# Kernel tuning notes

Measured on AMD Instinct MI355X. Metric: run time of the kernel, lower is better.

The kernel has to match this reference:

```python
import jax, jax.numpy as jnp
import numpy as np

N_ATOMS = 65536
N_BONDS = 131072
N_MOLS = 512
D_IN = 16
D = 128
REPEAT = 3


def _dense(key, fan_in, fan_out):
    kw, kb = jax.random.split(key)
    scale = 1.0 / np.sqrt(fan_in)
    W = jax.random.normal(kw, (fan_in, fan_out), dtype=jnp.float32) * scale
    b = jnp.zeros((fan_out,), dtype=jnp.float32)
    return W, b


def setup_inputs() -> dict:
    key = jax.random.key(0)
    ks = jax.random.split(key, 12)
    atoms = jax.random.normal(ks[0], (N_ATOMS, D_IN), dtype=jnp.float32)
    bond_orders = jax.random.uniform(ks[1], (N_BONDS,), dtype=jnp.float32)
    bond_src = jax.random.randint(ks[2], (N_BONDS,), 0, N_ATOMS, dtype=jnp.int32)
    bond_dst = jax.random.randint(ks[3], (N_BONDS,), 0, N_ATOMS, dtype=jnp.int32)
    atom_mol = jnp.sort(jax.random.randint(ks[4], (N_ATOMS,), 0, N_MOLS, dtype=jnp.int32))
    bond_mol = jnp.sort(jax.random.randint(ks[5], (N_BONDS,), 0, N_MOLS, dtype=jnp.int32))
    W_fe, b_fe = _dense(ks[6], 1, D)      # f_e : bond order -> h_e
    W_fv, b_fv = _dense(ks[7], D_IN, D)   # f_v : atom feats -> h_v
    W_fu, b_fu = _dense(ks[8], D, D)      # f_u : per-mol init from aggregated nodes
    W_e, b_e = _dense(ks[9], 5 * D, D)    # phi_e(h_e, h_e0, h_left, h_right, u)
    W_v, b_v = _dense(ks[10], 4 * D, D)   # phi_v(h_v, h_v0, e_bar_i, u)
    W_u, b_u = _dense(ks[11], 4 * D, D)   # phi_u(h_u, h_u0, e_bar, v_bar)
    return dict(atoms=atoms, bond_orders=bond_orders, W_fe=W_fe, b_fe=b_fe,
                W_fv=W_fv, b_fv=b_fv, W_fu=W_fu, b_fu=b_fu, W_e=W_e, b_e=b_e,
                W_v=W_v, b_v=b_v, W_u=W_u, b_u=b_u,
                bond_src=bond_src, bond_dst=bond_dst,
                atom_mol=atom_mol, bond_mol=bond_mol)


def reference(atoms, bond_orders, W_fe, b_fe, W_fv, b_fv, W_fu, b_fu,
              W_e, b_e, W_v, b_v, W_u, b_u,
              bond_src, bond_dst, atom_mol, bond_mol):
    seg = lambda x, ids, n: jax.ops.segment_sum(x, ids, num_segments=n)
    relu = jax.nn.relu

    # f_e / f_v / f_u initial embeddings
    h_e0 = relu(bond_orders[:, None] @ W_fe + b_fe)           # [E, D]
    h_v0 = relu(atoms @ W_fv + b_fv)                          # [N, D]
    h_u0 = relu(seg(h_v0, atom_mol, N_MOLS) @ W_fu + b_fu)    # [M, D]

    h_e, h_v, h_u = h_e0, h_v0, h_u0
    for _ in range(REPEAT):
        # phi_e(e_k, e_k_0, v_rk, v_sk, u): gather endpoints and per-bond global
        h_left = h_v[bond_src]                                # [E, D]
        h_right = h_v[bond_dst]                               # [E, D]
        u_e = h_u[bond_mol]                                   # [E, D]
        h_e = relu(jnp.concatenate([h_e, h_e0, h_left, h_right, u_e], axis=1) @ W_e + b_e)
        # rho_e_v: sum of updated edges incident to each atom (one-hot mask == scatter-add)
        e_bar_i = seg(h_e, bond_src, N_ATOMS) + seg(h_e, bond_dst, N_ATOMS)  # [N, D]
        # phi_v(v_i, v_i_0, e_bar_i, u)
        h_v = relu(jnp.concatenate([h_v, h_v0, e_bar_i, h_u[atom_mol]], axis=1) @ W_v + b_v)
        # rho_e_u / rho_v_u: per-molecule segment sums
        e_bar = seg(h_e, bond_mol, N_MOLS)                    # [M, D]
        v_bar = seg(h_v, atom_mol, N_MOLS)                    # [M, D]
        # phi_u(u, u_0, e_bar, v_bar)
        h_u = relu(jnp.concatenate([h_u, h_u0, e_bar, v_bar], axis=1) @ W_u + b_u)
    return h_u
```

## Files before the change

### kernel.cpp

```cpp
#include <hip/hip_runtime.h>
#include <hip/hip_bf16.h>
#include <stdint.h>

#define N_ATOMS 65536
#define N_BONDS 131072
#define N_MOLS  512
#define D_IN    16
#define DD      128
#define REPEAT  3
#define PITCH   136

typedef __attribute__((ext_vector_type(8))) short s8b;
typedef __attribute__((ext_vector_type(4))) float f32x4;

__device__ __forceinline__ float us2f(unsigned short s) {
    unsigned int u = ((unsigned int)s) << 16;
    float f; __builtin_memcpy(&f, &u, 4); return f;
}
__device__ __forceinline__ unsigned short f2us(float f) {
    __hip_bfloat16 h = __float2bfloat16(f);
    unsigned short s; __builtin_memcpy(&s, &h, 2); return s;
}
__device__ __forceinline__ void acc8(float* a, uint4 v) {
    unsigned short w[8]; __builtin_memcpy(w, &v, 16);
#pragma unroll
    for (int j = 0; j < 8; j++) a[j] += us2f(w[j]);
}


__device__ __forceinline__ void pack_one(const float* W, unsigned short* Wpk, int idx) {
    int k = idx >> 7, n = idx & 127;
    int c = k >> 7, ks = (k >> 5) & 3, quad = (k >> 3) & 3, j = k & 7;
    Wpk[(((c * 4 + ks) * 4 + quad) * 128 + n) * 8 + j] = f2us(W[k * 128 + n]);
}
__global__ void k_pack2(const float* __restrict__ We, const float* __restrict__ Wv,
                        unsigned short* __restrict__ WeP, unsigned short* __restrict__ WvP) {
    int idx = blockIdx.x * 256 + threadIdx.x;
    const int NE = 640 * 128;
    if (idx < NE) pack_one(We, WeP, idx);
    else if (idx < NE + 512 * 128) pack_one(Wv, WvP, idx - NE);
}

__global__ void k_deg(const int* __restrict__ bsrc, const int* __restrict__ bdst,
                      int* __restrict__ deg) {
    int e = blockIdx.x * 256 + threadIdx.x;
    atomicAdd(&deg[bsrc[e]], 1);
    atomicAdd(&deg[bdst[e]], 1);
}

__global__ void k_scan1(const int* __restrict__ deg, int* __restrict__ bsum) {
    __shared__ int red[256];
    int t = threadIdx.x;
    red[t] = deg[blockIdx.x * 256 + t];
    __syncthreads();
    for (int s = 128; s > 0; s >>= 1) {
        if (t < s) red[t] += red[t + s];
        __syncthreads();
    }
    if (t == 0) bsum[blockIdx.x] = red[0];
}

__global__ void k_scan3b(const int* __restrict__ deg, const int* __restrict__ bsum,
                         int* __restrict__ rowptr, int* __restrict__ cursor) {
    __shared__ int sb[256];
    __shared__ int s[256];
    int t = threadIdx.x;
    sb[t] = bsum[t];
    __syncthreads();
    for (int off = 1; off < 256; off <<= 1) {
        int v = (t >= off) ? sb[t - off] : 0;
        __syncthreads();
        sb[t] += v;
        __syncthreads();
    }
    int boff = sb[blockIdx.x] - bsum[blockIdx.x];
    int i = blockIdx.x * 256 + t;
    int d = deg[i];
    s[t] = d;
    __syncthreads();
    for (int off = 1; off < 256; off <<= 1) {
        int v = (t >= off) ? s[t - off] : 0;
        __syncthreads();
        s[t] += v;
        __syncthreads();
    }
    int val = boff + s[t] - d;
    rowptr[i] = val;
    cursor[i] = val;
    if (i == N_ATOMS - 1) rowptr[N_ATOMS] = val + d;
}

__global__ void k_fill(const int* __restrict__ bsrc, const int* __restrict__ bdst,
                       int* __restrict__ cursor, int* __restrict__ adj) {
    int e = blockIdx.x * 256 + threadIdx.x;
    int p = atomicAdd(&cursor[bsrc[e]], 1); adj[p] = e;
    int q = atomicAdd(&cursor[bdst[e]], 1); adj[q] = e;
}

__global__ void k_molptr2(const int* __restrict__ bmol, const int* __restrict__ amol,
                          int* __restrict__ bptr, int* __restrict__ aptr) {
    int m = threadIdx.x;
    if (m > N_MOLS) return;
    const int* ids = blockIdx.x ? amol : bmol;
    int rows = blockIdx.x ? N_ATOMS : N_BONDS;
    int* out = blockIdx.x ? aptr : bptr;
    int lo = 0, hi = rows;
    while (lo < hi) {
        int mid = (lo + hi) >> 1;
        if (ids[mid] < m) lo = mid + 1; else hi = mid;
    }
    out[m] = lo;
}


__global__ __launch_bounds__(256) void k_molsum_s(const unsigned short* __restrict__ x,
                                                  const int* __restrict__ mptr,
                                                  float* __restrict__ out, int S) {
    __shared__ float red[16 * 128];
    int m = blockIdx.x / S, s = blockIdx.x - m * S;
    int b = mptr[m], e = mptr[m + 1];
    int len = (e - b + S - 1) / S;
    int r0 = b + s * len;
    int r1 = min(r0 + len, e);
    int rl = threadIdx.x >> 4, g = threadIdx.x & 15;
    float acc[8] = {0,0,0,0,0,0,0,0};
    for (int r = r0 + rl; r < r1; r += 16)
        acc8(acc, *reinterpret_cast<const uint4*>(x + (size_t)r * DD + g * 8));
#pragma unroll
    for (int j = 0; j < 8; j++) red[rl * 128 + g * 8 + j] = acc[j];
    __syncthreads();
    if (threadIdx.x < 128) {
        int col = threadIdx.x;
        float sum = 0.f;
#pragma unroll
        for (int i = 0; i < 16; i++) sum += red[i * 128 + col];
        atomicAdd(&out[(size_t)m * DD + col], sum);
    }
}

__global__ __launch_bounds__(256) void k_mol_init_f(
        const float* __restrict__ ns, const float* __restrict__ Wfu,
        const float* __restrict__ bfu,
        const float* __restrict__ We, const float* __restrict__ be,
        const float* __restrict__ Wv, const float* __restrict__ bv,
        float* __restrict__ hu0, float* __restrict__ yue, float* __restrict__ yuv) {
    __shared__ float hrow[2 * DD];
    int tid = threadIdx.x;
    int ml = tid >> 7, d = tid & 127;
    int m = blockIdx.x * 2 + ml;
    float acc = bfu[d];
    for (int k = 0; k < DD; k++)
        acc = fmaf(ns[m*DD + k], Wfu[k*DD + d], acc);
    float v = fmaxf(acc, 0.f);
    hu0[m*DD + d] = v;
    hrow[ml*DD + d] = v;
    __syncthreads();
    float ae = be[d], av = bv[d];
    for (int k = 0; k < DD; k++) {
        float h = hrow[ml*DD + k];
        ae = fmaf(h, We[(512 + k)*DD + d], ae);
        av = fmaf(h, Wv[(384 + k)*DD + d], av);
    }
    yue[m*DD + d] = ae;
    yuv[m*DD + d] = av;
}

__global__ __launch_bounds__(256) void k_ye0(
        const float* __restrict__ bo, const float* __restrict__ Wfe,
        const float* __restrict__ bfe, const unsigned short* __restrict__ Wpk,
        unsigned short* __restrict__ he, unsigned short* __restrict__ ye0) {
    __shared__ __align__(16) unsigned short xs[128 * PITCH];
    __shared__ float sbo[128];
    int tid = threadIdx.x;
    int e0 = blockIdx.x * 128;
    if (tid < 128) sbo[tid] = bo[e0 + tid];
    int wv = tid >> 6, lane = tid & 63, quad = lane >> 4, l15 = lane & 15;
    f32x4 acc[8][2];
#pragma unroll
    for (int mt = 0; mt < 8; mt++) {
        acc[mt][0] = (f32x4){0.f,0.f,0.f,0.f};
        acc[mt][1] = (f32x4){0.f,0.f,0.f,0.f};
    }
    __syncthreads();
    for (int t = 0; t < 8; t++) {
        int u = tid + t * 256;
        int i = u >> 4, g = (u & 15) * 8;
        float b = sbo[i];
        unsigned short tmp[8];
#pragma unroll
        for (int j = 0; j < 8; j++)
            tmp[j] = f2us(fmaxf(fmaf(b, Wfe[g + j], bfe[g + j]), 0.f));
        uint4 val; __builtin_memcpy(&val, tmp, 16);
        *reinterpret_cast<uint4*>(&xs[i * PITCH + g]) = val;
        *reinterpret_cast<uint4*>(he + (size_t)(e0 + i) * DD + g) = val;
    }
    __syncthreads();
#pragma unroll
    for (int ks = 0; ks < 4; ks++) {
        const unsigned short* wb = Wpk + ((1 * 4 + ks) * 4 + quad) * 1024 + (wv * 32 + l15) * 8;
        s8b b0 = *reinterpret_cast<const s8b*>(wb);
        s8b b1 = *reinterpret_cast<const s8b*>(wb + 128);
#pragma unroll
        for (int mt = 0; mt < 8; mt++) {
            s8b afr = *reinterpret_cast<const s8b*>(&xs[(mt*16 + l15) * PITCH + ks*32 + quad*8]);
            acc[mt][0] = __builtin_amdgcn_mfma_f32_16x16x32_bf16(afr, b0, acc[mt][0], 0, 0, 0);
            acc[mt][1] = __builtin_amdgcn_mfma_f32_16x16x32_bf16(afr, b1, acc[mt][1], 0, 0, 0);
        }
    }
#pragma unroll
    for (int mt = 0; mt < 8; mt++)
#pragma unroll
        for (int r = 0; r < 4; r++) {
            int row = e0 + mt*16 + quad*4 + r;
#pragma unroll
            for (int nt = 0; nt < 2; nt++) {
                int col = wv*32 + nt*16 + l15;
                ye0[(size_t)row * DD + col] = f2us(acc[mt][nt][r]);
            }
        }
}

__global__ __launch_bounds__(256) void k_nodes_f(
        const float* __restrict__ atoms, const float* __restrict__ Wfv,
        const float* __restrict__ bfv, const unsigned short* __restrict__ Wpk,
        unsigned short* __restrict__ hv, unsigned short* __restrict__ yv0,
        float* __restrict__ node_sum) {
    __shared__ __align__(16) unsigned short xs[128 * PITCH];
    int tid = threadIdx.x;
    int gid = blockIdx.x * 256 + tid;
    if (gid < N_MOLS * DD) node_sum[gid] = 0.f;
    int n0 = blockIdx.x * 128;
    int wv = tid >> 6, lane = tid & 63, quad = lane >> 4, l15 = lane & 15;
    f32x4 acc[8][2];
#pragma unroll
    for (int mt = 0; mt < 8; mt++) {
        acc[mt][0] = (f32x4){0.f,0.f,0.f,0.f};
        acc[mt][1] = (f32x4){0.f,0.f,0.f,0.f};
    }
    for (int t = 0; t < 8; t++) {
        int u = tid + t * 256;
        int i = u >> 4, g = (u & 15) * 8;
        int row = n0 + i;
        float a[D_IN];
#pragma unroll
        for (int k = 0; k < D_IN; k++) a[k] = atoms[(size_t)row * D_IN + k];
        unsigned short tmp[8];
#pragma unroll
        for (int j = 0; j < 8; j++) {
            float acc1 = bfv[g + j];
#pragma unroll
            for (int k = 0; k < D_IN; k++)
                acc1 = fmaf(a[k], Wfv[k*DD + g + j], acc1);
            tmp[j] = f2us(fmaxf(acc1, 0.f));
        }
        uint4 val; __builtin_memcpy(&val, tmp, 16);
        *reinterpret_cast<uint4*>(&xs[i * PITCH + g]) = val;
        *reinterpret_cast<uint4*>(hv + (size_t)row * DD + g) = val;
    }
    __syncthreads();
#pragma unroll
    for (int ks = 0; ks < 4; ks++) {
        const unsigned short* wb = Wpk + ((1 * 4 + ks) * 4 + quad) * 1024 + (wv * 32 + l15) * 8;
        s8b b0 = *reinterpret_cast<const s8b*>(wb);
        s8b b1 = *reinterpret_cast<const s8b*>(wb + 128);
#pragma unroll
        for (int mt = 0; mt < 8; mt++) {
            s8b afr = *reinterpret_cast<const s8b*>(&xs[(mt*16 + l15) * PITCH + ks*32 + quad*8]);
            acc[mt][0] = __builtin_amdgcn_mfma_f32_16x16x32_bf16(afr, b0, acc[mt][0], 0, 0, 0);
            acc[mt][1] = __builtin_amdgcn_mfma_f32_16x16x32_bf16(afr, b1, acc[mt][1], 0, 0, 0);
        }
    }
#pragma unroll
    for (int mt = 0; mt < 8; mt++)
#pragma unroll
        for (int r = 0; r < 4; r++) {
            int row = n0 + mt*16 + quad*4 + r;
#pragma unroll
            for (int nt = 0; nt < 2; nt++) {
                int col = wv*32 + nt*16 + l15;
                yv0[(size_t)row * DD + col] = f2us(acc[mt][nt][r]);
            }
        }
}

__global__ __launch_bounds__(256) void k_zsd(
        const unsigned short* __restrict__ hv, const unsigned short* __restrict__ Wpk,
        unsigned short* __restrict__ Zs, unsigned short* __restrict__ Zd,
        float* __restrict__ ebar, float* __restrict__ vbar) {
    __shared__ __align__(16) unsigned short xs[128 * PITCH];
    int tid = threadIdx.x;
    int gid = blockIdx.x * 256 + tid;
    if (gid < N_MOLS * DD) ebar[gid] = 0.f;
    else                   vbar[gid - N_MOLS * DD] = 0.f;
    int n0 = blockIdx.x * 128;
    int wv = tid >> 6, lane = tid & 63, quad = lane >> 4, l15 = lane & 15;
    f32x4 aS[8][2], aD[8][2];
#pragma unroll
    for (int mt = 0; mt < 8; mt++) {
        aS[mt][0] = (f32x4){0.f,0.f,0.f,0.f}; aS[mt][1] = (f32x4){0.f,0.f,0.f,0.f};
        aD[mt][0] = (f32x4){0.f,0.f,0.f,0.f}; aD[mt][1] = (f32x4){0.f,0.f,0.f,0.f};
    }
    for (int t = 0; t < 8; t++) {
        int u = tid + t * 256;
        int i = u >> 4, g = (u & 15) * 8;
        *reinterpret_cast<uint4*>(&xs[i * PITCH + g]) =
            *reinterpret_cast<const uint4*>(hv + (size_t)(n0 + i) * DD + g);
    }
    __syncthreads();
#pragma unroll
    for (int ks = 0; ks < 4; ks++) {
        const unsigned short* wbS = Wpk + ((2 * 4 + ks) * 4 + quad) * 1024 + (wv * 32 + l15) * 8;
        const unsigned short* wbD = Wpk + ((3 * 4 + ks) * 4 + quad) * 1024 + (wv * 32 + l15) * 8;
        s8b s0 = *reinterpret_cast<const s8b*>(wbS);
        s8b s1 = *reinterpret_cast<const s8b*>(wbS + 128);
        s8b d0 = *reinterpret_cast<const s8b*>(wbD);
        s8b d1 = *reinterpret_cast<const s8b*>(wbD + 128);
#pragma unroll
        for (int mt = 0; mt < 8; mt++) {
            s8b afr = *reinterpret_cast<const s8b*>(&xs[(mt*16 + l15) * PITCH + ks*32 + quad*8]);
            aS[mt][0] = __builtin_amdgcn_mfma_f32_16x16x32_bf16(afr, s0, aS[mt][0], 0, 0, 0);
            aS[mt][1] = __builtin_amdgcn_mfma_f32_16x16x32_bf16(afr, s1, aS[mt][1], 0, 0, 0);
            aD[mt][0] = __builtin_amdgcn_mfma_f32_16x16x32_bf16(afr, d0, aD[mt][0], 0, 0, 0);
            aD[mt][1] = __builtin_amdgcn_mfma_f32_16x16x32_bf16(afr, d1, aD[mt][1], 0, 0, 0);
        }
    }
#pragma unroll
    for (int mt = 0; mt < 8; mt++)
#pragma unroll
        for (int r = 0; r < 4; r++) {
            int row = n0 + mt*16 + quad*4 + r;
#pragma unroll
            for (int nt = 0; nt < 2; nt++) {
                int col = wv*32 + nt*16 + l15;
                Zs[(size_t)row * DD + col] = f2us(aS[mt][nt][r]);
                Zd[(size_t)row * DD + col] = f2us(aD[mt][nt][r]);
            }
        }
}

__global__ __launch_bounds__(256) void k_phi_e(
        unsigned short* __restrict__ he, const unsigned short* __restrict__ ye0,
        const unsigned short* __restrict__ Zs, const unsigned short* __restrict__ Zd,
        const unsigned short* __restrict__ Wpk, const float* __restrict__ yue,
        const int* __restrict__ bsrc, const int* __restrict__ bdst,
        const int* __restrict__ bmol, float* __restrict__ ebar) {
    __shared__ __align__(16) unsigned short xs[128 * PITCH];
    __shared__ int ssrc[128], sdst[128], smol[128];
    int tid = threadIdx.x;
    int e0 = blockIdx.x * 128;
    if (tid < 128) {
        ssrc[tid] = bsrc[e0 + tid];
        sdst[tid] = bdst[e0 + tid];
        smol[tid] = bmol[e0 + tid];
    }
    int wv = tid >> 6, lane = tid & 63, quad = lane >> 4, l15 = lane & 15;
    f32x4 acc[8][2];
#pragma unroll
    for (int mt = 0; mt < 8; mt++) {
        acc[mt][0] = (f32x4){0.f,0.f,0.f,0.f};
        acc[mt][1] = (f32x4){0.f,0.f,0.f,0.f};
    }
    for (int t = 0; t < 8; t++) {
        int u = tid + t * 256;
        int i = u >> 4, g = (u & 15) * 8;
        *reinterpret_cast<uint4*>(&xs[i * PITCH + g]) =
            *reinterpret_cast<const uint4*>(he + (size_t)(e0 + i) * DD + g);
    }
    __syncthreads();
#pragma unroll
    for (int ks = 0; ks < 4; ks++) {
        const unsigned short* wb = Wpk + ((0 * 4 + ks) * 4 + quad) * 1024 + (wv * 32 + l15) * 8;
        s8b b0 = *reinterpret_cast<const s8b*>(wb);
        s8b b1 = *reinterpret_cast<const s8b*>(wb + 128);
#pragma unroll
        for (int mt = 0; mt < 8; mt++) {
            s8b afr = *reinterpret_cast<const s8b*>(&xs[(mt*16 + l15) * PITCH + ks*32 + quad*8]);
            acc[mt][0] = __builtin_amdgcn_mfma_f32_16x16x32_bf16(afr, b0, acc[mt][0], 0, 0, 0);
            acc[mt][1] = __builtin_amdgcn_mfma_f32_16x16x32_bf16(afr, b1, acc[mt][1], 0, 0, 0);
        }
    }
    __syncthreads();
    for (int t = 0; t < 8; t++) {
        int u = tid + t * 256;
        int i = u >> 4, g = (u & 15) * 8;
        float s[8] = {0,0,0,0,0,0,0,0};
        acc8(s, *reinterpret_cast<const uint4*>(ye0 + (size_t)(e0 + i) * DD + g));
        acc8(s, *reinterpret_cast<const uint4*>(Zs  + (size_t)ssrc[i] * DD + g));
        acc8(s, *reinterpret_cast<const uint4*>(Zd  + (size_t)sdst[i] * DD + g));
        const float* yr = yue + (size_t)smol[i] * DD + g;
        float4 y0 = *reinterpret_cast<const float4*>(yr);
        float4 y1 = *reinterpret_cast<const float4*>(yr + 4);
        s[0] += y0.x; s[1] += y0.y; s[2] += y0.z; s[3] += y0.w;
        s[4] += y1.x; s[5] += y1.y; s[6] += y1.z; s[7] += y1.w;
        unsigned short tmp[8];
#pragma unroll
        for (int j = 0; j < 8; j++) tmp[j] = f2us(s[j]);
        uint4 val; __builtin_memcpy(&val, tmp, 16);
        *reinterpret_cast<uint4*>(&xs[i * PITCH + g]) = val;
    }
    __syncthreads();
#pragma unroll
    for (int nt = 0; nt < 2; nt++) {
        int col = wv*32 + nt*16 + l15;
        float run = 0.f;
        int cur = smol[quad * 4];
#pragma unroll
        for (int mt = 0; mt < 8; mt++)
#pragma unroll
            for (int r = 0; r < 4; r++) {
                int rl = mt*16 + quad*4 + r;
                float v = fmaxf(acc[mt][nt][r] + us2f(xs[rl * PITCH + col]), 0.f);
                he[(size_t)(e0 + rl) * DD + col] = f2us(v);
                int m = smol[rl];
                if (m != cur) { atomicAdd(&ebar[(size_t)cur * DD + col], run); run = 0.f; cur = m; }
                run += v;
            }
        atomicAdd(&ebar[(size_t)cur * DD + col], run);
    }
}

__global__ __launch_bounds__(256) void k_phi_v(
        unsigned short* __restrict__ hv, const unsigned short* __restrict__ he,
        const int* __restrict__ rowptr, const int* __restrict__ adj,
        const unsigned short* __restrict__ yv0,
        const unsigned short* __restrict__ Wpk, const float* __restrict__ yuv,
        const int* __restrict__ amol, float* __restrict__ vbar) {
    __shared__ __align__(16) unsigned short xs[128 * PITCH];
    __shared__ int smol[128];
    int tid = threadIdx.x;
    int n0 = blockIdx.x * 128;
    if (tid < 128) smol[tid] = amol[n0 + tid];
    int wv = tid >> 6, lane = tid & 63, quad = lane >> 4, l15 = lane & 15;
    f32x4 acc[8][2];
#pragma unroll
    for (int mt = 0; mt < 8; mt++) {
        acc[mt][0] = (f32x4){0.f,0.f,0.f,0.f};
        acc[mt][1] = (f32x4){0.f,0.f,0.f,0.f};
    }
    for (int t = 0; t < 8; t++) {
        int u = tid + t * 256;
        int i = u >> 4, g = (u & 15) * 8;
        *reinterpret_cast<uint4*>(&xs[i * PITCH + g]) =
            *reinterpret_cast<const uint4*>(hv + (size_t)(n0 + i) * DD + g);
    }
    __syncthreads();
#pragma unroll
    for (int ks = 0; ks < 4; ks++) {
        const unsigned short* wb = Wpk + ((0 * 4 + ks) * 4 + quad) * 1024 + (wv * 32 + l15) * 8;
        s8b b0 = *reinterpret_cast<const s8b*>(wb);
        s8b b1 = *reinterpret_cast<const s8b*>(wb + 128);
#pragma unroll
        for (int mt = 0; mt < 8; mt++) {
            s8b afr = *reinterpret_cast<const s8b*>(&xs[(mt*16 + l15) * PITCH + ks*32 + quad*8]);
            acc[mt][0] = __builtin_amdgcn_mfma_f32_16x16x32_bf16(afr, b0, acc[mt][0], 0, 0, 0);
            acc[mt][1] = __builtin_amdgcn_mfma_f32_16x16x32_bf16(afr, b1, acc[mt][1], 0, 0, 0);
        }
    }
    __syncthreads();
    {
        int g = tid & 15, ab = tid >> 4;
#pragma unroll
        for (int k = 0; k < 8; k++) {
            int a = ab + 16 * k;
            int n = n0 + a;
            int b = rowptr[n], e = rowptr[n + 1];
            float s[8] = {0,0,0,0,0,0,0,0};
            int j = b;
            for (; j + 1 < e; j += 2) {
                uint4 v0 = *reinterpret_cast<const uint4*>(he + (size_t)adj[j]     * DD + g * 8);
                uint4 v1 = *reinterpret_cast<const uint4*>(he + (size_t)adj[j + 1] * DD + g * 8);
                acc8(s, v0); acc8(s, v1);
            }
            if (j < e)
                acc8(s, *reinterpret_cast<const uint4*>(he + (size_t)adj[j] * DD + g * 8));
            unsigned short tmp[8];
#pragma unroll
            for (int jj = 0; jj < 8; jj++) tmp[jj] = f2us(s[jj]);
            uint4 val; __builtin_memcpy(&val, tmp, 16);
            *reinterpret_cast<uint4*>(&xs[a * PITCH + g * 8]) = val;
        }
    }
    __syncthreads();
#pragma unroll
    for (int ks = 0; ks < 4; ks++) {
        const unsigned short* wb = Wpk + ((2 * 4 + ks) * 4 + quad) * 1024 + (wv * 32 + l15) * 8;
        s8b b0 = *reinterpret_cast<const s8b*>(wb);
        s8b b1 = *reinterpret_cast<const s8b*>(wb + 128);
#pragma unroll
        for (int mt = 0; mt < 8; mt++) {
            s8b afr = *reinterpret_cast<const s8b*>(&xs[(mt*16 + l15) * PITCH + ks*32 + quad*8]);
            acc[mt][0] = __builtin_amdgcn_mfma_f32_16x16x32_bf16(afr, b0, acc[mt][0], 0, 0, 0);
            acc[mt][1] = __builtin_amdgcn_mfma_f32_16x16x32_bf16(afr, b1, acc[mt][1], 0, 0, 0);
        }
    }
    __syncthreads();
    for (int t = 0; t < 8; t++) {
        int u = tid + t * 256;
        int i = u >> 4, g = (u & 15) * 8;
        float s[8] = {0,0,0,0,0,0,0,0};
        acc8(s, *reinterpret_cast<const uint4*>(yv0 + (size_t)(n0 + i) * DD + g));
        const float* yr = yuv + (size_t)smol[i] * DD + g;
        float4 y0 = *reinterpret_cast<const float4*>(yr);
        float4 y1 = *reinterpret_cast<const float4*>(yr + 4);
        s[0] += y0.x; s[1] += y0.y; s[2] += y0.z; s[3] += y0.w;
        s[4] += y1.x; s[5] += y1.y; s[6] += y1.z; s[7] += y1.w;
        unsigned short tmp[8];
#pragma unroll
        for (int j = 0; j < 8; j++) tmp[j] = f2us(s[j]);
        uint4 val; __builtin_memcpy(&val, tmp, 16);
        *reinterpret_cast<uint4*>(&xs[i * PITCH + g]) = val;
    }
    __syncthreads();
#pragma unroll
    for (int nt = 0; nt < 2; nt++) {
        int col = wv*32 + nt*16 + l15;
        float run = 0.f;
        int cur = smol[quad * 4];
#pragma unroll
        for (int mt = 0; mt < 8; mt++)
#pragma unroll
            for (int r = 0; r < 4; r++) {
                int rl = mt*16 + quad*4 + r;
                float v = fmaxf(acc[mt][nt][r] + us2f(xs[rl * PITCH + col]), 0.f);
                hv[(size_t)(n0 + rl) * DD + col] = f2us(v);
                int m = smol[rl];
                if (m != cur) { atomicAdd(&vbar[(size_t)cur * DD + col], run); run = 0.f; cur = m; }
                run += v;
            }
        atomicAdd(&vbar[(size_t)cur * DD + col], run);
    }
}

__global__ __launch_bounds__(256) void k_phi_u_f(
        const float* __restrict__ hu_in, const float* __restrict__ hu0,
        const float* __restrict__ ebar, const float* __restrict__ vbar,
        const float* __restrict__ Wu, const float* __restrict__ bu,
        const float* __restrict__ We, const float* __restrict__ be,
        const float* __restrict__ Wv, const float* __restrict__ bv,
        float* __restrict__ hu_out, float* __restrict__ dout,
        float* __restrict__ yue, float* __restrict__ yuv) {
    __shared__ float hrow[2 * DD];
    int tid = threadIdx.x;
    int ml = tid >> 7, d = tid & 127;
    int m = blockIdx.x * 2 + ml;
    float acc = bu[d];
    const float* segs[4] = { hu_in + m*DD, hu0 + m*DD, ebar + m*DD, vbar + m*DD };
    for (int s = 0; s < 4; s++) {
        const float* x = segs[s];
        const float* W = Wu + (s*DD)*DD + d;
        for (int k = 0; k < DD; k++)
            acc = fmaf(x[k], W[k*DD], acc);
    }
    float v = fmaxf(acc, 0.f);
    hu_out[m*DD + d] = v;
    dout[m*DD + d] = v;
    hrow[ml*DD + d] = v;
    __syncthreads();
    float ae = be[d], av = bv[d];
    for (int k = 0; k < DD; k++) {
        float h = hrow[ml*DD + k];
        ae = fmaf(h, We[(512 + k)*DD + d], ae);
        av = fmaf(h, Wv[(384 + k)*DD + d], av);
    }
    yue[m*DD + d] = ae;
    yuv[m*DD + d] = av;
}


extern "C" void kernel_launch(void* const* d_in, const int* in_sizes, int n_in,
                              void* d_out, int out_size, void* d_ws, size_t ws_size,
                              hipStream_t stream) {
    const float* atoms = (const float*)d_in[0];
    const float* bo    = (const float*)d_in[1];
    const float* Wfe   = (const float*)d_in[2];
    const float* bfe   = (const float*)d_in[3];
    const float* Wfv   = (const float*)d_in[4];
    const float* bfv   = (const float*)d_in[5];
    const float* Wfu   = (const float*)d_in[6];
    const float* bfu   = (const float*)d_in[7];
    const float* We    = (const float*)d_in[8];
    const float* be    = (const float*)d_in[9];
    const float* Wv    = (const float*)d_in[10];
    const float* bv    = (const float*)d_in[11];
    const float* Wu    = (const float*)d_in[12];
    const float* bu    = (const float*)d_in[13];
    const int* bsrc    = (const int*)d_in[14];
    const int* bdst    = (const int*)d_in[15];
    const int* amol    = (const int*)d_in[16];
    const int* bmol    = (const int*)d_in[17];

    char* p = (char*)d_ws;
    auto alloc = [&](size_t bytes) {
        char* r = p;
        p += (bytes + 255) & ~(size_t)255;
        return r;
    };
    unsigned short* he     = (unsigned short*)alloc((size_t)N_BONDS * DD * 2);
    unsigned short* ye0    = (unsigned short*)alloc((size_t)N_BONDS * DD * 2);
    unsigned short* hv     = (unsigned short*)alloc((size_t)N_ATOMS * DD * 2);
    unsigned short* yv0    = (unsigned short*)alloc((size_t)N_ATOMS * DD * 2);
    unsigned short* Zs     = (unsigned short*)alloc((size_t)N_ATOMS * DD * 2);
    unsigned short* Zd     = (unsigned short*)alloc((size_t)N_ATOMS * DD * 2);
    unsigned short* WeP    = (unsigned short*)alloc((size_t)640 * DD * 2);
    unsigned short* WvP    = (unsigned short*)alloc((size_t)512 * DD * 2);
    int* deg      = (int*)alloc((size_t)N_ATOMS * 4);
    int* rowptr   = (int*)alloc((size_t)(N_ATOMS + 1) * 4);
    int* cursor   = (int*)alloc((size_t)N_ATOMS * 4);
    int* adj      = (int*)alloc((size_t)2 * N_BONDS * 4);
    int* bmol_ptr = (int*)alloc((size_t)(N_MOLS + 1) * 4);
    int* amol_ptr = (int*)alloc((size_t)(N_MOLS + 1) * 4);
    int* bsum     = (int*)alloc((size_t)256 * 4);
    float* node_sum = (float*)alloc((size_t)N_MOLS * DD * 4);
    float* hu0   = (float*)alloc((size_t)N_MOLS * DD * 4);
    float* huA   = (float*)alloc((size_t)N_MOLS * DD * 4);
    float* huB   = (float*)alloc((size_t)N_MOLS * DD * 4);
    float* ebar  = (float*)alloc((size_t)N_MOLS * DD * 4);
    float* vbar  = (float*)alloc((size_t)N_MOLS * DD * 4);
    float* yue   = (float*)alloc((size_t)N_MOLS * DD * 4);
    float* yuv   = (float*)alloc((size_t)N_MOLS * DD * 4);

    hipMemsetAsync(deg, 0, (size_t)N_ATOMS * 4, stream);
    k_deg<<<N_BONDS/256, 256, 0, stream>>>(bsrc, bdst, deg);
    k_scan1<<<256, 256, 0, stream>>>(deg, bsum);
    k_scan3b<<<256, 256, 0, stream>>>(deg, bsum, rowptr, cursor);
    k_fill<<<N_BONDS/256, 256, 0, stream>>>(bsrc, bdst, cursor, adj);
    k_molptr2<<<2, 1024, 0, stream>>>(bmol, amol, bmol_ptr, amol_ptr);

    k_pack2<<<(640*DD + 512*DD)/256, 256, 0, stream>>>(We, Wv, WeP, WvP);

    k_ye0<<<N_BONDS/128, 256, 0, stream>>>(bo, Wfe, bfe, WeP, he, ye0);
    k_nodes_f<<<N_ATOMS/128, 256, 0, stream>>>(atoms, Wfv, bfv, WvP, hv, yv0, node_sum);
    k_molsum_s<<<N_MOLS*2, 256, 0, stream>>>(hv, amol_ptr, node_sum, 2);
    k_mol_init_f<<<N_MOLS/2, 256, 0, stream>>>(node_sum, Wfu, bfu, We, be, Wv, bv,
                                               hu0, yue, yuv);

    const float* hu_in = hu0; float* hu_out = huA;

    for (int r = 0; r < REPEAT; r++) {
        k_zsd<<<N_ATOMS/128, 256, 0, stream>>>(hv, WeP, Zs, Zd, ebar, vbar);
        k_phi_e<<<N_BONDS/128, 256, 0, stream>>>(he, ye0, Zs, Zd, WeP, yue,
                                                 bsrc, bdst, bmol, ebar);
        k_phi_v<<<N_ATOMS/128, 256, 0, stream>>>(hv, he, rowptr, adj, yv0, WvP, yuv,
                                                 amol, vbar);
        k_phi_u_f<<<N_MOLS/2, 256, 0, stream>>>(hu_in, hu0, ebar, vbar, Wu, bu,
                                                We, be, Wv, bv,
                                                hu_out, (float*)d_out, yue, yuv);
        hu_in = hu_out; hu_out = (hu_out == huA) ? huB : huA;
    }
}
```

Baseline: 537.7 us.

## Fuse Zs/Zd projection into node kernels, recompute ye0 in phi_e, split edge aggregation

Drops the separate k_zsd kernel: the source/destination projections of h_v are computed in k_nodes_f for the first iteration and at the end of k_phi_v for later ones, reusing the h_v tile already in shared memory. The stored ye0 buffer is removed; k_phi_e recomputes h_e0 from bond orders and runs an extra MFMA pass, trading compute for 32 MB of reads per iteration. The per-atom incident-edge sum moves into its own k_ebar kernel with 4-way unrolled gathers, and k_phi_v now reads that bf16 result. The ebar/vbar zeroing moves into the molecule kernels.

Result: faster. 498.6 us (-7.3%).

```diff
diff --git a/kernel.cpp b/kernel.cpp
--- a/kernel.cpp
+++ b/kernel.cpp
@@ -25,6 +25,41 @@
     unsigned short w[8]; __builtin_memcpy(w, &v, 16);
 #pragma unroll
     for (int j = 0; j < 8; j++) a[j] += us2f(w[j]);
+}
+
+__device__ __forceinline__ void mfma_store(const unsigned short* xs,
+        const unsigned short* __restrict__ Wpk, int wc,
+        unsigned short* __restrict__ out, int row0, int tid) {
+    int wv = tid >> 6, lane = tid & 63, quad = lane >> 4, l15 = lane & 15;
+    f32x4 acc[8][2];
+#pragma unroll
+    for (int mt = 0; mt < 8; mt++) {
+        acc[mt][0] = (f32x4){0.f,0.f,0.f,0.f};
+        acc[mt][1] = (f32x4){0.f,0.f,0.f,0.f};
+    }
+#pragma unroll
+    for (int ks = 0; ks < 4; ks++) {
+        const unsigned short* wb = Wpk + ((wc * 4 + ks) * 4 + quad) * 1024 + (wv * 32 + l15) * 8;
+        s8b b0 = *reinterpret_cast<const s8b*>(wb);
+        s8b b1 = *reinterpret_cast<const s8b*>(wb + 128);
+#pragma unroll
+        for (int mt = 0; mt < 8; mt++) {
+            s8b afr = *reinterpret_cast<const s8b*>(&xs[(mt*16 + l15) * PITCH + ks*32 + quad*8]);
+            acc[mt][0] = __builtin_amdgcn_mfma_f32_16x16x32_bf16(afr, b0, acc[mt][0], 0, 0, 0);
+            acc[mt][1] = __builtin_amdgcn_mfma_f32_16x16x32_bf16(afr, b1, acc[mt][1], 0, 0, 0);
+        }
+    }
+#pragma unroll
+    for (int mt = 0; mt < 8; mt++)
+#pragma unroll
+        for (int r = 0; r < 4; r++) {
+            int row = row0 + mt*16 + quad*4 + r;
+#pragma unroll
+            for (int nt = 0; nt < 2; nt++) {
+                int col = wv*32 + nt*16 + l15;
+                out[(size_t)row * DD + col] = f2us(acc[mt][nt][r]);
+            }
+        }
 }
 
 
@@ -112,6 +147,51 @@
     out[m] = lo;
 }
 
+
+__global__ void k_init_he(const float* __restrict__ bo, const float* __restrict__ Wfe,
+                          const float* __restrict__ bfe, unsigned short* __restrict__ he) {
+    int idx = blockIdx.x * 256 + threadIdx.x;
+    int e = idx >> 7, d = idx & 127;
+    he[idx] = f2us(fmaxf(fmaf(bo[e], Wfe[d], bfe[d]), 0.f));
+}
+
+__global__ __launch_bounds__(256) void k_nodes_f(
+        const float* __restrict__ atoms, const float* __restrict__ Wfv,
+        const float* __restrict__ bfv,
+        const unsigned short* __restrict__ WvP, const unsigned short* __restrict__ WeP,
+        unsigned short* __restrict__ hv, unsigned short* __restrict__ yv0,
+        unsigned short* __restrict__ Zs, unsigned short* __restrict__ Zd,
+        float* __restrict__ node_sum) {
+    __shared__ __align__(16) unsigned short xs[128 * PITCH];
+    int tid = threadIdx.x;
+    int gid = blockIdx.x * 256 + tid;
+    if (gid < N_MOLS * DD) node_sum[gid] = 0.f;
+    int n0 = blockIdx.x * 128;
+    for (int t = 0; t < 8; t++) {
+        int u = tid + t * 256;
+        int i = u >> 4, g = (u & 15) * 8;
+        int row = n0 + i;
+        float a[D_IN];
+#pragma unroll
+        for (int k = 0; k < D_IN; k++) a[k] = atoms[(size_t)row * D_IN + k];
+        unsigned short tmp[8];
+#pragma unroll
+        for (int j = 0; j < 8; j++) {
+            float acc1 = bfv[g + j];
+#pragma unroll
+            for (int k = 0; k < D_IN; k++)
+                acc1 = fmaf(a[k], Wfv[k*DD + g + j], acc1);
+            tmp[j] = f2us(fmaxf(acc1, 0.f));
+        }
+        uint4 val; __builtin_memcpy(&val, tmp, 16);
+        *reinterpret_cast<uint4*>(&xs[i * PITCH + g]) = val;
+        *reinterpret_cast<uint4*>(hv + (size_t)row * DD + g) = val;
+    }
+    __syncthreads();
+    mfma_store(xs, WvP, 1, yv0, n0, tid);
+    mfma_store(xs, WeP, 2, Zs, n0, tid);
+    mfma_store(xs, WeP, 3, Zd, n0, tid);
+}
 
 __global__ __launch_bounds__(256) void k_molsum_s(const unsigned short* __restrict__ x,
                                                   const int* __restrict__ mptr,
@@ -143,11 +223,14 @@
         const float* __restrict__ bfu,
         const float* __restrict__ We, const float* __restrict__ be,
         const float* __restrict__ Wv, const float* __restrict__ bv,
-        float* __restrict__ hu0, float* __restrict__ yue, float* __restrict__ yuv) {
+        float* __restrict__ hu0, float* __restrict__ yue, float* __restrict__ yuv,
+        float* __restrict__ ebar, float* __restrict__ vbar) {
     __shared__ float hrow[2 * DD];
     int tid = threadIdx.x;
     int ml = tid >> 7, d = tid & 127;
     int m = blockIdx.x * 2 + ml;
+    ebar[m*DD + d] = 0.f;
+    vbar[m*DD + d] = 0.f;
     float acc = bfu[d];
     for (int k = 0; k < DD; k++)
         acc = fmaf(ns[m*DD + k], Wfu[k*DD + d], acc);
@@ -165,193 +248,24 @@
     yuv[m*DD + d] = av;
 }
 
-__global__ __launch_bounds__(256) void k_ye0(
+__global__ __launch_bounds__(256) void k_phi_e(
+        unsigned short* __restrict__ he,
         const float* __restrict__ bo, const float* __restrict__ Wfe,
-        const float* __restrict__ bfe, const unsigned short* __restrict__ Wpk,
-        unsigned short* __restrict__ he, unsigned short* __restrict__ ye0) {
-    __shared__ __align__(16) unsigned short xs[128 * PITCH];
-    __shared__ float sbo[128];
-    int tid = threadIdx.x;
-    int e0 = blockIdx.x * 128;
-    if (tid < 128) sbo[tid] = bo[e0 + tid];
-    int wv = tid >> 6, lane = tid & 63, quad = lane >> 4, l15 = lane & 15;
-    f32x4 acc[8][2];
-#pragma unroll
-    for (int mt = 0; mt < 8; mt++) {
-        acc[mt][0] = (f32x4){0.f,0.f,0.f,0.f};
-        acc[mt][1] = (f32x4){0.f,0.f,0.f,0.f};
-    }
-    __syncthreads();
-    for (int t = 0; t < 8; t++) {
-        int u = tid + t * 256;
-        int i = u >> 4, g = (u & 15) * 8;
-        float b = sbo[i];
-        unsigned short tmp[8];
-#pragma unroll
-        for (int j = 0; j < 8; j++)
-            tmp[j] = f2us(fmaxf(fmaf(b, Wfe[g + j], bfe[g + j]), 0.f));
-        uint4 val; __builtin_memcpy(&val, tmp, 16);
-        *reinterpret_cast<uint4*>(&xs[i * PITCH + g]) = val;
-        *reinterpret_cast<uint4*>(he + (size_t)(e0 + i) * DD + g) = val;
-    }
-    __syncthreads();
-#pragma unroll
-    for (int ks = 0; ks < 4; ks++) {
-        const unsigned short* wb = Wpk + ((1 * 4 + ks) * 4 + quad) * 1024 + (wv * 32 + l15) * 8;
-        s8b b0 = *reinterpret_cast<const s8b*>(wb);
-        s8b b1 = *reinterpret_cast<const s8b*>(wb + 128);
-#pragma unroll
-        for (int mt = 0; mt < 8; mt++) {
-            s8b afr = *reinterpret_cast<const s8b*>(&xs[(mt*16 + l15) * PITCH + ks*32 + quad*8]);
-            acc[mt][0] = __builtin_amdgcn_mfma_f32_16x16x32_bf16(afr, b0, acc[mt][0], 0, 0, 0);
-            acc[mt][1] = __builtin_amdgcn_mfma_f32_16x16x32_bf16(afr, b1, acc[mt][1], 0, 0, 0);
-        }
-    }
-#pragma unroll
-    for (int mt = 0; mt < 8; mt++)
-#pragma unroll
-        for (int r = 0; r < 4; r++) {
-            int row = e0 + mt*16 + quad*4 + r;
-#pragma unroll
-            for (int nt = 0; nt < 2; nt++) {
-                int col = wv*32 + nt*16 + l15;
-                ye0[(size_t)row * DD + col] = f2us(acc[mt][nt][r]);
-            }
-        }
-}
-
-__global__ __launch_bounds__(256) void k_nodes_f(
-        const float* __restrict__ atoms, const float* __restrict__ Wfv,
-        const float* __restrict__ bfv, const unsigned short* __restrict__ Wpk,
-        unsigned short* __restrict__ hv, unsigned short* __restrict__ yv0,
-        float* __restrict__ node_sum) {
-    __shared__ __align__(16) unsigned short xs[128 * PITCH];
-    int tid = threadIdx.x;
-    int gid = blockIdx.x * 256 + tid;
-    if (gid < N_MOLS * DD) node_sum[gid] = 0.f;
-    int n0 = blockIdx.x * 128;
-    int wv = tid >> 6, lane = tid & 63, quad = lane >> 4, l15 = lane & 15;
-    f32x4 acc[8][2];
-#pragma unroll
-    for (int mt = 0; mt < 8; mt++) {
-        acc[mt][0] = (f32x4){0.f,0.f,0.f,0.f};
-        acc[mt][1] = (f32x4){0.f,0.f,0.f,0.f};
-    }
-    for (int t = 0; t < 8; t++) {
-        int u = tid + t * 256;
-        int i = u >> 4, g = (u & 15) * 8;
-        int row = n0 + i;
-        float a[D_IN];
-#pragma unroll
-        for (int k = 0; k < D_IN; k++) a[k] = atoms[(size_t)row * D_IN + k];
-        unsigned short tmp[8];
-#pragma unroll
-        for (int j = 0; j < 8; j++) {
-            float acc1 = bfv[g + j];
-#pragma unroll
-            for (int k = 0; k < D_IN; k++)
-                acc1 = fmaf(a[k], Wfv[k*DD + g + j], acc1);
-            tmp[j] = f2us(fmaxf(acc1, 0.f));
-        }
-        uint4 val; __builtin_memcpy(&val, tmp, 16);
-        *reinterpret_cast<uint4*>(&xs[i * PITCH + g]) = val;
-        *reinterpret_cast<uint4*>(hv + (size_t)row * DD + g) = val;
-    }
-    __syncthreads();
-#pragma unroll
-    for (int ks = 0; ks < 4; ks++) {
-        const unsigned short* wb = Wpk + ((1 * 4 + ks) * 4 + quad) * 1024 + (wv * 32 + l15) * 8;
-        s8b b0 = *reinterpret_cast<const s8b*>(wb);
-        s8b b1 = *reinterpret_cast<const s8b*>(wb + 128);
-#pragma unroll
-        for (int mt = 0; mt < 8; mt++) {
-            s8b afr = *reinterpret_cast<const s8b*>(&xs[(mt*16 + l15) * PITCH + ks*32 + quad*8]);
-            acc[mt][0] = __builtin_amdgcn_mfma_f32_16x16x32_bf16(afr, b0, acc[mt][0], 0, 0, 0);
-            acc[mt][1] = __builtin_amdgcn_mfma_f32_16x16x32_bf16(afr, b1, acc[mt][1], 0, 0, 0);
-        }
-    }
-#pragma unroll
-    for (int mt = 0; mt < 8; mt++)
-#pragma unroll
-        for (int r = 0; r < 4; r++) {
-            int row = n0 + mt*16 + quad*4 + r;
-#pragma unroll
-            for (int nt = 0; nt < 2; nt++) {
-                int col = wv*32 + nt*16 + l15;
-                yv0[(size_t)row * DD + col] = f2us(acc[mt][nt][r]);
-            }
-        }
-}
-
-__global__ __launch_bounds__(256) void k_zsd(
-        const unsigned short* __restrict__ hv, const unsigned short* __restrict__ Wpk,
-        unsigned short* __restrict__ Zs, unsigned short* __restrict__ Zd,
-        float* __restrict__ ebar, float* __restrict__ vbar) {
-    __shared__ __align__(16) unsigned short xs[128 * PITCH];
-    int tid = threadIdx.x;
-    int gid = blockIdx.x * 256 + tid;
-    if (gid < N_MOLS * DD) ebar[gid] = 0.f;
-    else                   vbar[gid - N_MOLS * DD] = 0.f;
-    int n0 = blockIdx.x * 128;
-    int wv = tid >> 6, lane = tid & 63, quad = lane >> 4, l15 = lane & 15;
-    f32x4 aS[8][2], aD[8][2];
-#pragma unroll
-    for (int mt = 0; mt < 8; mt++) {
-        aS[mt][0] = (f32x4){0.f,0.f,0.f,0.f}; aS[mt][1] = (f32x4){0.f,0.f,0.f,0.f};
-        aD[mt][0] = (f32x4){0.f,0.f,0.f,0.f}; aD[mt][1] = (f32x4){0.f,0.f,0.f,0.f};
-    }
-    for (int t = 0; t < 8; t++) {
-        int u = tid + t * 256;
-        int i = u >> 4, g = (u & 15) * 8;
-        *reinterpret_cast<uint4*>(&xs[i * PITCH + g]) =
-            *reinterpret_cast<const uint4*>(hv + (size_t)(n0 + i) * DD + g);
-    }
-    __syncthreads();
-#pragma unroll
-    for (int ks = 0; ks < 4; ks++) {
-        const unsigned short* wbS = Wpk + ((2 * 4 + ks) * 4 + quad) * 1024 + (wv * 32 + l15) * 8;
-        const unsigned short* wbD = Wpk + ((3 * 4 + ks) * 4 + quad) * 1024 + (wv * 32 + l15) * 8;
-        s8b s0 = *reinterpret_cast<const s8b*>(wbS);
-        s8b s1 = *reinterpret_cast<const s8b*>(wbS + 128);
-        s8b d0 = *reinterpret_cast<const s8b*>(wbD);
-        s8b d1 = *reinterpret_cast<const s8b*>(wbD + 128);
-#pragma unroll
-        for (int mt = 0; mt < 8; mt++) {
-            s8b afr = *reinterpret_cast<const s8b*>(&xs[(mt*16 + l15) * PITCH + ks*32 + quad*8]);
-            aS[mt][0] = __builtin_amdgcn_mfma_f32_16x16x32_bf16(afr, s0, aS[mt][0], 0, 0, 0);
-            aS[mt][1] = __builtin_amdgcn_mfma_f32_16x16x32_bf16(afr, s1, aS[mt][1], 0, 0, 0);
-            aD[mt][0] = __builtin_amdgcn_mfma_f32_16x16x32_bf16(afr, d0, aD[mt][0], 0, 0, 0);
-            aD[mt][1] = __builtin_amdgcn_mfma_f32_16x16x32_bf16(afr, d1, aD[mt][1], 0, 0, 0);
-        }
-    }
-#pragma unroll
-    for (int mt = 0; mt < 8; mt++)
-#pragma unroll
-        for (int r = 0; r < 4; r++) {
-            int row = n0 + mt*16 + quad*4 + r;
-#pragma unroll
-            for (int nt = 0; nt < 2; nt++) {
-                int col = wv*32 + nt*16 + l15;
-                Zs[(size_t)row * DD + col] = f2us(aS[mt][nt][r]);
-                Zd[(size_t)row * DD + col] = f2us(aD[mt][nt][r]);
-            }
-        }
-}
-
-__global__ __launch_bounds__(256) void k_phi_e(
-        unsigned short* __restrict__ he, const unsigned short* __restrict__ ye0,
+        const float* __restrict__ bfe,
         const unsigned short* __restrict__ Zs, const unsigned short* __restrict__ Zd,
         const unsigned short* __restrict__ Wpk, const float* __restrict__ yue,
         const int* __restrict__ bsrc, const int* __restrict__ bdst,
         const int* __restrict__ bmol, float* __restrict__ ebar) {
     __shared__ __align__(16) unsigned short xs[128 * PITCH];
     __shared__ int ssrc[128], sdst[128], smol[128];
+    __shared__ float sbo[128];
     int tid = threadIdx.x;
     int e0 = blockIdx.x * 128;
     if (tid < 128) {
         ssrc[tid] = bsrc[e0 + tid];
         sdst[tid] = bdst[e0 + tid];
         smol[tid] = bmol[e0 + tid];
+        sbo[tid]  = bo[e0 + tid];
     }
     int wv = tid >> 6, lane = tid & 63, quad = lane >> 4, l15 = lane & 15;
     f32x4 acc[8][2];
@@ -383,10 +297,34 @@
     for (int t = 0; t < 8; t++) {
         int u = tid + t * 256;
         int i = u >> 4, g = (u & 15) * 8;
+        float b = sbo[i];
+        unsigned short tmp[8];
+#pragma unroll
+        for (int j = 0; j < 8; j++)
+            tmp[j] = f2us(fmaxf(fmaf(b, Wfe[g + j], bfe[g + j]), 0.f));
+        uint4 val; __builtin_memcpy(&val, tmp, 16);
+        *reinterpret_cast<uint4*>(&xs[i * PITCH + g]) = val;
+    }
+    __syncthreads();
+#pragma unroll
+    for (int ks = 0; ks < 4; ks++) {
+        const unsigned short* wb = Wpk + ((1 * 4 + ks) * 4 + quad) * 1024 + (wv * 32 + l15) * 8;
+        s8b b0 = *reinterpret_cast<const s8b*>(wb);
+        s8b b1 = *reinterpret_cast<const s8b*>(wb + 128);
+#pragma unroll
+        for (int mt = 0; mt < 8; mt++) {
+            s8b afr = *reinterpret_cast<const s8b*>(&xs[(mt*16 + l15) * PITCH + ks*32 + quad*8]);
+            acc[mt][0] = __builtin_amdgcn_mfma_f32_16x16x32_bf16(afr, b0, acc[mt][0], 0, 0, 0);
+            acc[mt][1] = __builtin_amdgcn_mfma_f32_16x16x32_bf16(afr, b1, acc[mt][1], 0, 0, 0);
+        }
+    }
+    __syncthreads();
+    for (int t = 0; t < 8; t++) {
+        int u = tid + t * 256;
+        int i = u >> 4, g = (u & 15) * 8;
         float s[8] = {0,0,0,0,0,0,0,0};
-        acc8(s, *reinterpret_cast<const uint4*>(ye0 + (size_t)(e0 + i) * DD + g));
-        acc8(s, *reinterpret_cast<const uint4*>(Zs  + (size_t)ssrc[i] * DD + g));
-        acc8(s, *reinterpret_cast<const uint4*>(Zd  + (size_t)sdst[i] * DD + g));
+        acc8(s, *reinterpret_cast<const uint4*>(Zs + (size_t)ssrc[i] * DD + g));
+        acc8(s, *reinterpret_cast<const uint4*>(Zd + (size_t)sdst[i] * DD + g));
         const float* yr = yue + (size_t)smol[i] * DD + g;
         float4 y0 = *reinterpret_cast<const float4*>(yr);
         float4 y1 = *reinterpret_cast<const float4*>(yr + 4);
@@ -419,12 +357,38 @@
     }
 }
 
+__global__ __launch_bounds__(256) void k_ebar(const unsigned short* __restrict__ he,
+                                              const int* __restrict__ rowptr,
+                                              const int* __restrict__ adj,
+                                              unsigned short* __restrict__ ebar_i) {
+    int n = blockIdx.x * 16 + (threadIdx.x >> 4);
+    int g = threadIdx.x & 15;
+    int b = rowptr[n], e = rowptr[n + 1];
+    float acc[8] = {0,0,0,0,0,0,0,0};
+    int j = b;
+    for (; j + 3 < e; j += 4) {
+        uint4 v0 = *reinterpret_cast<const uint4*>(he + (size_t)adj[j]     * DD + g * 8);
+        uint4 v1 = *reinterpret_cast<const uint4*>(he + (size_t)adj[j + 1] * DD + g * 8);
+        uint4 v2 = *reinterpret_cast<const uint4*>(he + (size_t)adj[j + 2] * DD + g * 8);
+        uint4 v3 = *reinterpret_cast<const uint4*>(he + (size_t)adj[j + 3] * DD + g * 8);
+        acc8(acc, v0); acc8(acc, v1); acc8(acc, v2); acc8(acc, v3);
+    }
+    for (; j < e; j++)
+        acc8(acc, *reinterpret_cast<const uint4*>(he + (size_t)adj[j] * DD + g * 8));
+    unsigned short o[8];
+#pragma unroll
+    for (int k = 0; k < 8; k++) o[k] = f2us(acc[k]);
+    uint4 ov; __builtin_memcpy(&ov, o, 16);
+    *reinterpret_cast<uint4*>(ebar_i + (size_t)n * DD + g * 8) = ov;
+}
+
 __global__ __launch_bounds__(256) void k_phi_v(
-        unsigned short* __restrict__ hv, const unsigned short* __restrict__ he,
-        const int* __restrict__ rowptr, const int* __restrict__ adj,
+        unsigned short* __restrict__ hv, const unsigned short* __restrict__ ebar_i,
         const unsigned short* __restrict__ yv0,
-        const unsigned short* __restrict__ Wpk, const float* __restrict__ yuv,
-        const int* __restrict__ amol, float* __restrict__ vbar) {
+        const unsigned short* __restrict__ WvP, const unsigned short* __restrict__ WeP,
+        const float* __restrict__ yuv, const int* __restrict__ amol,
+        float* __restrict__ vbar,
+        unsigned short* __restrict__ Zs, unsigned short* __restrict__ Zd, int do_z) {
     __shared__ __align__(16) unsigned short xs[128 * PITCH];
     __shared__ int smol[128];
     int tid = threadIdx.x;
@@ -437,60 +401,29 @@
         acc[mt][0] = (f32x4){0.f,0.f,0.f,0.f};
         acc[mt][1] = (f32x4){0.f,0.f,0.f,0.f};
     }
-    for (int t = 0; t < 8; t++) {
-        int u = tid + t * 256;
-        int i = u >> 4, g = (u & 15) * 8;
-        *reinterpret_cast<uint4*>(&xs[i * PITCH + g]) =
-            *reinterpret_cast<const uint4*>(hv + (size_t)(n0 + i) * DD + g);
-    }
-    __syncthreads();
-#pragma unroll
-    for (int ks = 0; ks < 4; ks++) {
-        const unsigned short* wb = Wpk + ((0 * 4 + ks) * 4 + quad) * 1024 + (wv * 32 + l15) * 8;
-        s8b b0 = *reinterpret_cast<const s8b*>(wb);
-        s8b b1 = *reinterpret_cast<const s8b*>(wb + 128);
-#pragma unroll
-        for (int mt = 0; mt < 8; mt++) {
-            s8b afr = *reinterpret_cast<const s8b*>(&xs[(mt*16 + l15) * PITCH + ks*32 + quad*8]);
-            acc[mt][0] = __builtin_amdgcn_mfma_f32_16x16x32_bf16(afr, b0, acc[mt][0], 0, 0, 0);
-            acc[mt][1] = __builtin_amdgcn_mfma_f32_16x16x32_bf16(afr, b1, acc[mt][1], 0, 0, 0);
-        }
-    }
-    __syncthreads();
-    {
-        int g = tid & 15, ab = tid >> 4;
-#pragma unroll
-        for (int k = 0; k < 8; k++) {
-            int a = ab + 16 * k;
-            int n = n0 + a;
-            int b = rowptr[n], e = rowptr[n + 1];
-            float s[8] = {0,0,0,0,0,0,0,0};
-            int j = b;
-            for (; j + 1 < e; j += 2) {
-                uint4 v0 = *reinterpret_cast<const uint4*>(he + (size_t)adj[j]     * DD + g * 8);
-                uint4 v1 = *reinterpret_cast<const uint4*>(he + (size_t)adj[j + 1] * DD + g * 8);
-                acc8(s, v0); acc8(s, v1);
+    const unsigned short* bases[2] = { hv + (size_t)n0 * DD, ebar_i + (size_t)n0 * DD };
+    const int wcs[2] = {0, 2};
+    for (int c = 0; c < 2; c++) {
+        if (c) __syncthreads();
+        for (int t = 0; t < 8; t++) {
+            int u = tid + t * 256;
+            int i = u >> 4, g = (u & 15) * 8;
+            *reinterpret_cast<uint4*>(&xs[i * PITCH + g]) =
+                *reinterpret_cast<const uint4*>(bases[c] + (size_t)i * DD + g);
+        }
+        __syncthreads();
+        int WC = wcs[c];
+#pragma unroll
+        for (int ks = 0; ks < 4; ks++) {
+            const unsigned short* wb = WvP + ((WC * 4 + ks) * 4 + quad) * 1024 + (wv * 32 + l15) * 8;
+            s8b b0 = *reinterpret_cast<const s8b*>(wb);
+            s8b b1 = *reinterpret_cast<const s8b*>(wb + 128);
+#pragma unroll
+            for (int mt = 0; mt < 8; mt++) {
+                s8b afr = *reinterpret_cast<const s8b*>(&xs[(mt*16 + l15) * PITCH + ks*32 + quad*8]);
+                acc[mt][0] = __builtin_amdgcn_mfma_f32_16x16x32_bf16(afr, b0, acc[mt][0], 0, 0, 0);
+                acc[mt][1] = __builtin_amdgcn_mfma_f32_16x16x32_bf16(afr, b1, acc[mt][1], 0, 0, 0);
             }
-            if (j < e)
-                acc8(s, *reinterpret_cast<const uint4*>(he + (size_t)adj[j] * DD + g * 8));
-            unsigned short tmp[8];
-#pragma unroll
-            for (int jj = 0; jj < 8; jj++) tmp[jj] = f2us(s[jj]);
-            uint4 val; __builtin_memcpy(&val, tmp, 16);
-            *reinterpret_cast<uint4*>(&xs[a * PITCH + g * 8]) = val;
-        }
-    }
-    __syncthreads();
-#pragma unroll
-    for (int ks = 0; ks < 4; ks++) {
-        const unsigned short* wb = Wpk + ((2 * 4 + ks) * 4 + quad) * 1024 + (wv * 32 + l15) * 8;
-        s8b b0 = *reinterpret_cast<const s8b*>(wb);
-        s8b b1 = *reinterpret_cast<const s8b*>(wb + 128);
-#pragma unroll
-        for (int mt = 0; mt < 8; mt++) {
-            s8b afr = *reinterpret_cast<const s8b*>(&xs[(mt*16 + l15) * PITCH + ks*32 + quad*8]);
-            acc[mt][0] = __builtin_amdgcn_mfma_f32_16x16x32_bf16(afr, b0, acc[mt][0], 0, 0, 0);
-            acc[mt][1] = __builtin_amdgcn_mfma_f32_16x16x32_bf16(afr, b1, acc[mt][1], 0, 0, 0);
         }
     }
     __syncthreads();
@@ -522,18 +455,25 @@
             for (int r = 0; r < 4; r++) {
                 int rl = mt*16 + quad*4 + r;
                 float v = fmaxf(acc[mt][nt][r] + us2f(xs[rl * PITCH + col]), 0.f);
-                hv[(size_t)(n0 + rl) * DD + col] = f2us(v);
+                unsigned short vb = f2us(v);
+                hv[(size_t)(n0 + rl) * DD + col] = vb;
+                xs[rl * PITCH + col] = vb;
                 int m = smol[rl];
                 if (m != cur) { atomicAdd(&vbar[(size_t)cur * DD + col], run); run = 0.f; cur = m; }
                 run += v;
             }
         atomicAdd(&vbar[(size_t)cur * DD + col], run);
     }
+    if (do_z) {
+        __syncthreads();
+        mfma_store(xs, WeP, 2, Zs, n0, tid);
+        mfma_store(xs, WeP, 3, Zd, n0, tid);
+    }
 }
 
 __global__ __launch_bounds__(256) void k_phi_u_f(
         const float* __restrict__ hu_in, const float* __restrict__ hu0,
-        const float* __restrict__ ebar, const float* __restrict__ vbar,
+        float* __restrict__ ebar, float* __restrict__ vbar,
         const float* __restrict__ Wu, const float* __restrict__ bu,
         const float* __restrict__ We, const float* __restrict__ be,
         const float* __restrict__ Wv, const float* __restrict__ bv,
@@ -556,6 +496,8 @@
     dout[m*DD + d] = v;
     hrow[ml*DD + d] = v;
     __syncthreads();
+    ebar[m*DD + d] = 0.f;
+    vbar[m*DD + d] = 0.f;
     float ae = be[d], av = bv[d];
     for (int k = 0; k < DD; k++) {
         float h = hrow[ml*DD + k];
@@ -596,11 +538,11 @@
         return r;
     };
     unsigned short* he     = (unsigned short*)alloc((size_t)N_BONDS * DD * 2);
-    unsigned short* ye0    = (unsigned short*)alloc((size_t)N_BONDS * DD * 2);
     unsigned short* hv     = (unsigned short*)alloc((size_t)N_ATOMS * DD * 2);
     unsigned short* yv0    = (unsigned short*)alloc((size_t)N_ATOMS * DD * 2);
     unsigned short* Zs     = (unsigned short*)alloc((size_t)N_ATOMS * DD * 2);
     unsigned short* Zd     = (unsigned short*)alloc((size_t)N_ATOMS * DD * 2);
+    unsigned short* ebar_i = (unsigned short*)alloc((size_t)N_ATOMS * DD * 2);
     unsigned short* WeP    = (unsigned short*)alloc((size_t)640 * DD * 2);
     unsigned short* WvP    = (unsigned short*)alloc((size_t)512 * DD * 2);
     int* deg      = (int*)alloc((size_t)N_ATOMS * 4);
@@ -628,20 +570,21 @@
 
     k_pack2<<<(640*DD + 512*DD)/256, 256, 0, stream>>>(We, Wv, WeP, WvP);
 
-    k_ye0<<<N_BONDS/128, 256, 0, stream>>>(bo, Wfe, bfe, WeP, he, ye0);
-    k_nodes_f<<<N_ATOMS/128, 256, 0, stream>>>(atoms, Wfv, bfv, WvP, hv, yv0, node_sum);
+    k_init_he<<<(N_BONDS*DD)/256, 256, 0, stream>>>(bo, Wfe, bfe, he);
+    k_nodes_f<<<N_ATOMS/128, 256, 0, stream>>>(atoms, Wfv, bfv, WvP, WeP,
+                                               hv, yv0, Zs, Zd, node_sum);
     k_molsum_s<<<N_MOLS*2, 256, 0, stream>>>(hv, amol_ptr, node_sum, 2);
     k_mol_init_f<<<N_MOLS/2, 256, 0, stream>>>(node_sum, Wfu, bfu, We, be, Wv, bv,
-                                               hu0, yue, yuv);
+                                               hu0, yue, yuv, ebar, vbar);
 
     const float* hu_in = hu0; float* hu_out = huA;
 
     for (int r = 0; r < REPEAT; r++) {
-        k_zsd<<<N_ATOMS/128, 256, 0, stream>>>(hv, WeP, Zs, Zd, ebar, vbar);
-        k_phi_e<<<N_BONDS/128, 256, 0, stream>>>(he, ye0, Zs, Zd, WeP, yue,
+        k_phi_e<<<N_BONDS/128, 256, 0, stream>>>(he, bo, Wfe, bfe, Zs, Zd, WeP, yue,
                                                  bsrc, bdst, bmol, ebar);
-        k_phi_v<<<N_ATOMS/128, 256, 0, stream>>>(hv, he, rowptr, adj, yv0, WvP, yuv,
-                                                 amol, vbar);
+        k_ebar<<<N_ATOMS/16, 256, 0, stream>>>(he, rowptr, adj, ebar_i);
+        k_phi_v<<<N_ATOMS/128, 256, 0, stream>>>(hv, ebar_i, yv0, WvP, WeP, yuv,
+                                                 amol, vbar, Zs, Zd, (r < REPEAT - 1) ? 1 : 0);
         k_phi_u_f<<<N_MOLS/2, 256, 0, stream>>>(hu_in, hu0, ebar, vbar, Wu, bu,
                                                 We, be, Wv, bv,
                                                 hu_out, (float*)d_out, yue, yuv);
```
